# Kernel optimization log

Hardware: AMD Instinct MI355X
Metric: run time of the kernel (lower is better)

Reference implementation:

```python
import jax, jax.numpy as jnp
import numpy as np

N = 50000
E = 800000
T = 12
HID = 128
K = 3
F_IN = 7  # 1 (x) + 4 (env) + 2 (coords)
CIN = F_IN + HID  # DCRNN concatenates input with hidden state


def setup_inputs() -> dict:
    key = jax.random.key(0)
    ks = jax.random.split(key, 16)
    inp = {
        "x": jax.random.normal(ks[0], (N, T), dtype=jnp.float32),
        "env": jax.random.normal(ks[1], (N, 4, T), dtype=jnp.float32),
        "coords": jax.random.uniform(ks[2], (N, 2), dtype=jnp.float32),
        "edge_index": jax.random.randint(ks[3], (2, E), 0, N, dtype=jnp.int32),
        "edge_weight": jax.random.uniform(ks[4], (E,), dtype=jnp.float32),
        "local_night": jax.random.uniform(ks[5], (N, T + 1), dtype=jnp.float32),
        # DCRNN gate diffusion-conv weights: [2 (out/in direction), K, Cin, Cout]
        "Wz": jax.random.normal(ks[6], (2, K, CIN, HID), dtype=jnp.float32) * 0.05,
        "bz": jnp.zeros((HID,), dtype=jnp.float32),
        "Wr": jax.random.normal(ks[7], (2, K, CIN, HID), dtype=jnp.float32) * 0.05,
        "br": jnp.zeros((HID,), dtype=jnp.float32),
        "Wh": jax.random.normal(ks[8], (2, K, CIN, HID), dtype=jnp.float32) * 0.05,
        "bh": jnp.zeros((HID,), dtype=jnp.float32),
        "lin_W": jax.random.normal(ks[9], (HID, 1), dtype=jnp.float32) * 0.05,
        "lin_b": jnp.zeros((1,), dtype=jnp.float32),
    }
    return inp


def reference(x, env, coords, edge_weight, local_night, Wz, bz, Wr, br, Wh, bh, lin_W, lin_b, edge_index):
    row, col = edge_index[0], edge_index[1]
    n = x.shape[0]

    # out/in degrees of the weighted adjacency A[row, col] = w
    deg_out = jax.ops.segment_sum(edge_weight, row, num_segments=n)
    deg_in = jax.ops.segment_sum(edge_weight, col, num_segments=n)
    inv_out = jnp.where(deg_out > 0, 1.0 / deg_out, 0.0)
    inv_in = jnp.where(deg_in > 0, 1.0 / deg_in, 0.0)

    def prop_out(v):  # (D_O^{-1} A) v : gather from col, scatter-add to row
        msg = edge_weight[:, None] * v[col]
        return inv_out[:, None] * jax.ops.segment_sum(msg, row, num_segments=n)

    def prop_in(v):  # (D_I^{-1} A^T) v : gather from row, scatter-add to col
        msg = edge_weight[:, None] * v[row]
        return inv_in[:, None] * jax.ops.segment_sum(msg, col, num_segments=n)

    def dconv(X, W, b):
        # K-hop bidirectional diffusion convolution
        H = X @ (W[0, 0] + W[1, 0])
        Tx0 = X
        Tx_o = prop_out(X)
        Tx_i = prop_in(X)
        H = H + Tx_o @ W[0, 1] + Tx_i @ W[1, 1]
        for k in range(2, W.shape[1]):
            Tx_o = 2.0 * prop_out(Tx_o) - Tx0
            Tx_i = 2.0 * prop_in(Tx_i) - Tx0
            H = H + Tx_o @ W[0, k] + Tx_i @ W[1, k]
        return H + b

    env_t = jnp.moveaxis(env, -1, 0)          # [T, N, 4]
    night_t = jnp.transpose(local_night[:, 1:])  # [T, N]
    hid0 = jnp.zeros((n, HID), dtype=x.dtype)   # hidden state resets each call (H=None)

    def step(x_prev, ts):
        e, night = ts
        X = jnp.concatenate([x_prev, e, coords], axis=1)   # [N, 7]
        Xh = jnp.concatenate([X, hid0], axis=1)            # [N, 7+HID]
        Z = jax.nn.sigmoid(dconv(Xh, Wz, bz))
        R = jax.nn.sigmoid(dconv(Xh, Wr, br))  # H*R = 0 since H0 = 0; kept for fidelity
        H_tilde = jnp.tanh(dconv(Xh, Wh, bh))
        H_new = Z * hid0 + (1.0 - Z) * H_tilde
        out = jax.nn.relu(H_new) @ lin_W + lin_b           # [N, 1]
        out = out * night[:, None]
        return out, out

    x0 = x[:, 0:1]
    _, preds = jax.lax.scan(step, x0, (env_t, night_t))    # preds: [T, N, 1]
    predictions = jnp.concatenate([x0, jnp.transpose(preds[..., 0])], axis=1)  # [N, T+1]
    return predictions
```

## Files before the change

### kernel.cpp

```cpp
#include <hip/hip_runtime.h>
#include <hip/hip_fp16.h>

#define Nn 50000
#define Ee 800000
#define Tt 12
#define NBAND 8
#define BAND 6250
#define CAP 64

__global__ __launch_bounds__(256) void csr_direct(
    const int* __restrict__ ei, const float* __restrict__ ew,
    int* __restrict__ nextR, int* __restrict__ nextC,
    unsigned* __restrict__ adjR, unsigned* __restrict__ adjC)
{
    int band = blockIdx.x & (NBAND - 1);
    int chunk = blockIdx.x >> 3;
    int lo = band * BAND, hi = lo + BAND;
    int stride = (gridDim.x >> 3) * 256;
    for (int e = chunk * 256 + threadIdx.x; e < Ee; e += stride) {
        int r = ei[e], c = ei[Ee + e];
        bool br = (r >= lo) & (r < hi);
        bool bc = (c >= lo) & (c < hi);
        if (br | bc) {
            unsigned wb = __half_as_ushort(__float2half(ew[e]));
            if (br) adjR[(r << 6) + atomicAdd(&nextR[r], 1)] = ((unsigned)c << 16) | wb;
            if (bc) adjC[(c << 6) + atomicAdd(&nextC[c], 1)] = ((unsigned)r << 16) | wb;
        }
    }
}

__global__ __launch_bounds__(256) void weff_kernel(
    const float* __restrict__ Wz, const float* __restrict__ Wh,
    const float* __restrict__ bz, const float* __restrict__ bh,
    float* __restrict__ wzT, float* __restrict__ whT)
{
    int idx = blockIdx.x * 256 + threadIdx.x;
    if (idx >= 2 * 36 * 128) return;
    const float* W = (idx < 36 * 128) ? Wz : Wh;
    const float* B = (idx < 36 * 128) ? bz : bh;
    float* O       = (idx < 36 * 128) ? wzT : whT;
    int rem = idx % (36 * 128);
    int k = rem / 128, j = rem % 128;
    float v;
    if (k == 35) v = B[j];
    else {
        int p = k / 7, rr = k % 7;
        if (p == 0)      v = W[(0 * 135 + rr) * 128 + j] + W[(3 * 135 + rr) * 128 + j];
        else if (p == 1) v = W[(1 * 135 + rr) * 128 + j];
        else if (p == 2) v = W[(4 * 135 + rr) * 128 + j];
        else if (p == 3) v = W[(2 * 135 + rr) * 128 + j];
        else             v = W[(5 * 135 + rr) * 128 + j];
    }
    O[k * 128 + j] = v;
}

__global__ __launch_bounds__(256) void init_kernel(
    const float* __restrict__ x, const float* __restrict__ env,
    const float* __restrict__ coords, __half* __restrict__ Xh,
    float* __restrict__ out)
{
    int i = blockIdx.x * 256 + threadIdx.x;
    if (i >= Nn) return;
    float xv = x[i * Tt];
    __half* r = Xh + (long)i * 8;
    r[0] = __float2half(xv);
    #pragma unroll
    for (int c = 0; c < 4; c++) r[1 + c] = __float2half(env[i * 48 + c * 12]);
    r[5] = __float2half(coords[i * 2 + 0]);
    r[6] = __float2half(coords[i * 2 + 1]);
    r[7] = __half(0.f);
    out[i * 13 + 0] = xv;
}

__device__ __forceinline__ void unpack8(const __half* p, float* v) {
    uint4 hv = *((const uint4*)p);
    float2 p0 = __half22float2(*(__half2*)&hv.x);
    float2 p1 = __half22float2(*(__half2*)&hv.y);
    float2 p2 = __half22float2(*(__half2*)&hv.z);
    float2 p3 = __half22float2(*(__half2*)&hv.w);
    v[0] = p0.x; v[1] = p0.y; v[2] = p1.x; v[3] = p1.y;
    v[4] = p2.x; v[5] = p2.y; v[6] = p3.x;
}

__device__ __forceinline__ void pack8(__half* p, const float* v) {
    __half2 q0 = __floats2half2_rn(v[0], v[1]);
    __half2 q1 = __floats2half2_rn(v[2], v[3]);
    __half2 q2 = __floats2half2_rn(v[4], v[5]);
    __half2 q3 = __floats2half2_rn(v[6], 0.f);
    uint4 st;
    st.x = *(unsigned*)&q0; st.y = *(unsigned*)&q1;
    st.z = *(unsigned*)&q2; st.w = *(unsigned*)&q3;
    *((uint4*)p) = st;
}

__device__ __forceinline__ void acc7(float* a, float w, uint4 hv) {
    float2 p0 = __half22float2(*(__half2*)&hv.x);
    float2 p1 = __half22float2(*(__half2*)&hv.y);
    float2 p2 = __half22float2(*(__half2*)&hv.z);
    float2 p3 = __half22float2(*(__half2*)&hv.w);
    a[0] = fmaf(w, p0.x, a[0]); a[1] = fmaf(w, p0.y, a[1]);
    a[2] = fmaf(w, p1.x, a[2]); a[3] = fmaf(w, p1.y, a[3]);
    a[4] = fmaf(w, p2.x, a[4]); a[5] = fmaf(w, p2.y, a[5]);
    a[6] = fmaf(w, p3.x, a[6]);
}

__device__ __forceinline__ float wdec(unsigned ed) {
    return __half2float(__ushort_as_half((unsigned short)(ed & 0xffffu)));
}

__device__ __forceinline__ void gather6(
    const unsigned* __restrict__ adj, const __half* __restrict__ src,
    int b, int k0, int e, float* a, float* sw)
{
    unsigned en[6];
    bool v[6];
    #pragma unroll
    for (int s = 0; s < 6; s++) {
        int k = k0 + 4 * s;
        v[s] = k < e;
        en[s] = adj[v[s] ? k : b];
    }
    uint4 rv[6];
    #pragma unroll
    for (int s = 0; s < 6; s++)
        rv[s] = *(const uint4*)(src + (long)(v[s] ? (en[s] >> 16) : 0u) * 8);
    #pragma unroll
    for (int s = 0; s < 6; s++) {
        float w = v[s] ? wdec(en[s]) : 0.f;
        acc7(a, w, rv[s]);
        if (sw) *sw += w;
    }
    for (int k = k0 + 24; k < e; k += 4) {
        unsigned ed = adj[k];
        uint4 r2 = *(const uint4*)(src + (long)(ed >> 16) * 8);
        float w = wdec(ed);
        acc7(a, w, r2);
        if (sw) *sw += w;
    }
}

__global__ __launch_bounds__(256) void gather1_kernel(
    const int* __restrict__ cntR, const unsigned* __restrict__ adjR,
    const int* __restrict__ cntC, const unsigned* __restrict__ adjC,
    const __half* __restrict__ Xh,
    __half* __restrict__ TxoH, __half* __restrict__ TxiH,
    float* __restrict__ inv_out, float* __restrict__ inv_in)
{
    int tid = blockIdx.x * 256 + threadIdx.x;
    if (tid >= Nn * 8) return;
    int node = tid >> 3;
    int dir = (tid >> 2) & 1, sub = tid & 3;
    const int*      cn  = dir ? cntC : cntR;
    const unsigned* adj = dir ? adjC : adjR;
    int b = node << 6, e = b + cn[node];
    float a[7] = {0.f, 0.f, 0.f, 0.f, 0.f, 0.f, 0.f};
    float sw = 0.f;
    gather6(adj, Xh, b, b + sub, e, a, &sw);
    #pragma unroll
    for (int m = 1; m <= 2; m <<= 1) {
        #pragma unroll
        for (int q = 0; q < 7; q++) a[q] += __shfl_xor(a[q], m);
        sw += __shfl_xor(sw, m);
    }
    if (sub == 0) {
        float inv = sw > 0.f ? 1.f / sw : 0.f;
        (dir ? inv_in : inv_out)[node] = inv;
        #pragma unroll
        for (int q = 0; q < 7; q++) a[q] *= inv;
        pack8((dir ? TxiH : TxoH) + (long)node * 8, a);
    }
}

__global__ __launch_bounds__(256) void step2_kernel(
    const int* __restrict__ cntR, const unsigned* __restrict__ adjR,
    const int* __restrict__ cntC, const unsigned* __restrict__ adjC,
    const float* __restrict__ inv_out, const float* __restrict__ inv_in,
    const float* __restrict__ env, const float* __restrict__ night,
    const float* __restrict__ wzT, const float* __restrict__ whT,
    const float* __restrict__ linW, const float* __restrict__ linb,
    __half* __restrict__ Xh,
    const __half* __restrict__ TxoH, const __half* __restrict__ TxiH,
    float* __restrict__ out, int t)
{
    __shared__ float f_s[32][36];
    __shared__ float part_s[2][32];
    int tid = threadIdx.x;
    int base = blockIdx.x * 32;

    {
        int nl = tid >> 3;
        int dir = (tid >> 2) & 1, sub = tid & 3;
        int node = base + nl;
        int nc = node < Nn ? node : Nn - 1;
        const int*      cn  = dir ? cntC : cntR;
        const unsigned* adj = dir ? adjC : adjR;
        const __half*   src = dir ? TxiH : TxoH;
        int b = nc << 6, e = b + cn[nc];
        float a[7] = {0.f, 0.f, 0.f, 0.f, 0.f, 0.f, 0.f};
        gather6(adj, src, b, b + sub, e, a, nullptr);
        #pragma unroll
        for (int m = 1; m <= 2; m <<= 1) {
            #pragma unroll
            for (int q = 0; q < 7; q++) a[q] += __shfl_xor(a[q], m);
        }
        if (sub == 0) {
            float s2 = 2.f * (dir ? inv_in[nc] : inv_out[nc]);
            float xv[7], tx[7];
            unpack8(Xh + (long)nc * 8, xv);
            unpack8(src + (long)nc * 8, tx);
            #pragma unroll
            for (int q = 0; q < 7; q++) {
                f_s[nl][21 + 7 * dir + q] = fmaf(s2, a[q], -xv[q]);
                f_s[nl][7 + 7 * dir + q]  = tx[q];
            }
            if (dir == 0) {
                #pragma unroll
                for (int q = 0; q < 7; q++) f_s[nl][q] = xv[q];
                f_s[nl][35] = 1.f;
            }
        }
    }
    __syncthreads();

    int lane = tid & 63;
    int wave = tid >> 6;
    int chSel = wave & 1;
    int ch = chSel * 64 + lane;
    int half_id = wave >> 1;
    float wz[36], wh[36];
    #pragma unroll
    for (int k = 0; k < 36; k++) wz[k] = wzT[k * 128 + ch];
    #pragma unroll
    for (int k = 0; k < 36; k++) wh[k] = whT[k * 128 + ch];
    float lw = linW[ch];
    float lb = linb[0];

    #pragma unroll 1
    for (int n = 0; n < 16; n++) {
        int ni = half_id * 16 + n;
        const float4* fv = (const float4*)f_s[ni];
        float hz = 0.f, hh = 0.f;
        #pragma unroll
        for (int q = 0; q < 9; q++) {
            float4 fq = fv[q];
            hz = fmaf(fq.x, wz[q*4+0], hz); hh = fmaf(fq.x, wh[q*4+0], hh);
            hz = fmaf(fq.y, wz[q*4+1], hz); hh = fmaf(fq.y, wh[q*4+1], hh);
            hz = fmaf(fq.z, wz[q*4+2], hz); hh = fmaf(fq.z, wh[q*4+2], hh);
            hz = fmaf(fq.w, wz[q*4+3], hz); hh = fmaf(fq.w, wh[q*4+3], hh);
        }
        float z  = 1.f / (1.f + __expf(-hz));
        float e2 = __expf(2.f * hh);
        float ht = 1.f - 2.f / (e2 + 1.f);
        float v = fmaxf((1.f - z) * ht, 0.f) * lw;
        v += __shfl_xor(v, 1);  v += __shfl_xor(v, 2);  v += __shfl_xor(v, 4);
        v += __shfl_xor(v, 8);  v += __shfl_xor(v, 16); v += __shfl_xor(v, 32);
        if (lane == 0) part_s[chSel][ni] = v;
    }
    __syncthreads();
    if (tid < 32) {
        int node = base + tid;
        if (node < Nn) {
            float o = part_s[0][tid] + part_s[1][tid] + lb;
            o *= night[(long)node * 13 + t + 1];
            out[(long)node * 13 + t + 1] = o;
            if (t + 1 < Tt) {
                __half* xr = Xh + (long)node * 8;
                xr[0] = __float2half(o);
                #pragma unroll
                for (int c = 0; c < 4; c++)
                    xr[1 + c] = __float2half(env[(long)node * 48 + c * 12 + t + 1]);
            }
        }
    }
}

extern "C" void kernel_launch(void* const* d_in, const int* in_sizes, int n_in,
                              void* d_out, int out_size, void* d_ws, size_t ws_size,
                              hipStream_t stream) {
    const float* x      = (const float*)d_in[0];
    const float* env    = (const float*)d_in[1];
    const float* coords = (const float*)d_in[2];
    const int*   ei     = (const int*)d_in[3];
    const float* ew     = (const float*)d_in[4];
    const float* night  = (const float*)d_in[5];
    const float* Wz     = (const float*)d_in[6];
    const float* bz     = (const float*)d_in[7];
    const float* Wh     = (const float*)d_in[10];
    const float* bh     = (const float*)d_in[11];
    const float* linW   = (const float*)d_in[12];
    const float* linb   = (const float*)d_in[13];
    float* out = (float*)d_out;

    float* w = (float*)d_ws;
    float* wzT     = w;
    float* whT     = w + 4608;
    float* inv_out = w + 9216;
    float* inv_in  = w + 59216;
    __half* Xh   = (__half*)(w + 109216);
    __half* TxoH = (__half*)(w + 309216);
    __half* TxiH = (__half*)(w + 509216);
    int* nextR   = (int*)(w + 709216);
    int* nextC   = nextR + 50000;
    unsigned* adjR = (unsigned*)(w + 809216);
    unsigned* adjC = adjR + Nn * CAP;

    hipMemsetAsync(nextR, 0, 2 * Nn * sizeof(int), stream);
    csr_direct<<<8 * 256, 256, 0, stream>>>(ei, ew, nextR, nextC, adjR, adjC);

    weff_kernel<<<(2 * 36 * 128 + 255) / 256, 256, 0, stream>>>(Wz, Wh, bz, bh, wzT, whT);
    init_kernel<<<(Nn + 255) / 256, 256, 0, stream>>>(x, env, coords, Xh, out);

    for (int t = 0; t < Tt; t++) {
        gather1_kernel<<<(Nn * 8 + 255) / 256, 256, 0, stream>>>(
            nextR, adjR, nextC, adjC, Xh, TxoH, TxiH, inv_out, inv_in);
        step2_kernel<<<(Nn + 31) / 32, 256, 0, stream>>>(
            nextR, adjR, nextC, adjC, inv_out, inv_in,
            env, night, wzT, whT, linW, linb, Xh, TxoH, TxiH, out, t);
    }
}
```

Before: 700.7 us.

## Fuse time-step loop into persistent cooperative kernel with grid sync

Replaces the 24 per-step kernel launches with one cooperative persistent kernel. Inside it, blocks pull work items from atomic counters and separate the gather and step phases with grid-wide syncs. This targets launch overhead and tail gaps between the many small kernels. In exchange it adds grid.sync cost, atomic work-stealing overhead, and an occupancy limit from launch_bounds(256,4) with a grid capped at 4 blocks per CU. The old multi-launch path is kept as a fallback.

After: 703.5 us. No clear change (+0.4%).

```diff
diff --git a/kernel.cpp b/kernel.cpp
--- a/kernel.cpp
+++ b/kernel.cpp
@@ -1,5 +1,8 @@
 #include <hip/hip_runtime.h>
 #include <hip/hip_fp16.h>
+#include <hip/hip_cooperative_groups.h>
+
+namespace cg = cooperative_groups;
 
 #define Nn 50000
 #define Ee 800000
@@ -7,6 +10,8 @@
 #define NBAND 8
 #define BAND 6250
 #define CAP 64
+#define NCHUNK ((Nn * 8 + 255) / 256)
+#define NWI ((Nn + 31) / 32)
 
 __global__ __launch_bounds__(256) void csr_direct(
     const int* __restrict__ ei, const float* __restrict__ ew,
@@ -139,15 +144,14 @@
     }
 }
 
-__global__ __launch_bounds__(256) void gather1_kernel(
+__device__ __forceinline__ void gather_phase(
+    int tid,
     const int* __restrict__ cntR, const unsigned* __restrict__ adjR,
     const int* __restrict__ cntC, const unsigned* __restrict__ adjC,
     const __half* __restrict__ Xh,
     __half* __restrict__ TxoH, __half* __restrict__ TxiH,
     float* __restrict__ inv_out, float* __restrict__ inv_in)
 {
-    int tid = blockIdx.x * 256 + threadIdx.x;
-    if (tid >= Nn * 8) return;
     int node = tid >> 3;
     int dir = (tid >> 2) & 1, sub = tid & 3;
     const int*      cn  = dir ? cntC : cntR;
@@ -171,7 +175,8 @@
     }
 }
 
-__global__ __launch_bounds__(256) void step2_kernel(
+__device__ __forceinline__ void step_phase(
+    int wi, int t,
     const int* __restrict__ cntR, const unsigned* __restrict__ adjR,
     const int* __restrict__ cntC, const unsigned* __restrict__ adjC,
     const float* __restrict__ inv_out, const float* __restrict__ inv_in,
@@ -180,12 +185,12 @@
     const float* __restrict__ linW, const float* __restrict__ linb,
     __half* __restrict__ Xh,
     const __half* __restrict__ TxoH, const __half* __restrict__ TxiH,
-    float* __restrict__ out, int t)
+    float* __restrict__ out)
 {
     __shared__ float f_s[32][36];
     __shared__ float part_s[2][32];
     int tid = threadIdx.x;
-    int base = blockIdx.x * 32;
+    int base = wi * 32;
 
     {
         int nl = tid >> 3;
@@ -272,6 +277,73 @@
             }
         }
     }
+}
+
+__global__ __launch_bounds__(256, 4) void loop_kernel(
+    const int* __restrict__ cntR, const unsigned* __restrict__ adjR,
+    const int* __restrict__ cntC, const unsigned* __restrict__ adjC,
+    float* __restrict__ inv_out, float* __restrict__ inv_in,
+    const float* __restrict__ env, const float* __restrict__ night,
+    const float* __restrict__ wzT, const float* __restrict__ whT,
+    const float* __restrict__ linW, const float* __restrict__ linb,
+    __half* __restrict__ Xh, __half* __restrict__ TxoH, __half* __restrict__ TxiH,
+    float* __restrict__ out, int* __restrict__ ctr)
+{
+    cg::grid_group grid = cg::this_grid();
+    __shared__ int item_s;
+    for (int t = 0; t < Tt; t++) {
+        for (;;) {
+            if (threadIdx.x == 0) item_s = atomicAdd(&ctr[t], 1);
+            __syncthreads();
+            int chunk = item_s;
+            __syncthreads();
+            if (chunk >= NCHUNK) break;
+            int tid = chunk * 256 + threadIdx.x;
+            if (tid < Nn * 8)
+                gather_phase(tid, cntR, adjR, cntC, adjC, Xh, TxoH, TxiH,
+                             inv_out, inv_in);
+        }
+        __threadfence();
+        grid.sync();
+        for (;;) {
+            if (threadIdx.x == 0) item_s = atomicAdd(&ctr[12 + t], 1);
+            __syncthreads();
+            int wi = item_s;
+            __syncthreads();
+            if (wi >= NWI) break;
+            step_phase(wi, t, cntR, adjR, cntC, adjC, inv_out, inv_in,
+                       env, night, wzT, whT, linW, linb, Xh, TxoH, TxiH, out);
+        }
+        __threadfence();
+        grid.sync();
+    }
+}
+
+__global__ __launch_bounds__(256) void gather1_kernel(
+    const int* __restrict__ cntR, const unsigned* __restrict__ adjR,
+    const int* __restrict__ cntC, const unsigned* __restrict__ adjC,
+    const __half* __restrict__ Xh,
+    __half* __restrict__ TxoH, __half* __restrict__ TxiH,
+    float* __restrict__ inv_out, float* __restrict__ inv_in)
+{
+    int tid = blockIdx.x * 256 + threadIdx.x;
+    if (tid >= Nn * 8) return;
+    gather_phase(tid, cntR, adjR, cntC, adjC, Xh, TxoH, TxiH, inv_out, inv_in);
+}
+
+__global__ __launch_bounds__(256) void step2_kernel(
+    const int* __restrict__ cntR, const unsigned* __restrict__ adjR,
+    const int* __restrict__ cntC, const unsigned* __restrict__ adjC,
+    const float* __restrict__ inv_out, const float* __restrict__ inv_in,
+    const float* __restrict__ env, const float* __restrict__ night,
+    const float* __restrict__ wzT, const float* __restrict__ whT,
+    const float* __restrict__ linW, const float* __restrict__ linb,
+    __half* __restrict__ Xh,
+    const __half* __restrict__ TxoH, const __half* __restrict__ TxiH,
+    float* __restrict__ out, int t)
+{
+    step_phase(blockIdx.x, t, cntR, adjR, cntC, adjC, inv_out, inv_in,
+               env, night, wzT, whT, linW, linb, Xh, TxoH, TxiH, out);
 }
 
 extern "C" void kernel_launch(void* const* d_in, const int* in_sizes, int n_in,
@@ -301,20 +373,45 @@
     __half* TxiH = (__half*)(w + 509216);
     int* nextR   = (int*)(w + 709216);
     int* nextC   = nextR + 50000;
-    unsigned* adjR = (unsigned*)(w + 809216);
+    int* ctr     = (int*)(w + 809216);
+    unsigned* adjR = (unsigned*)(w + 809280);
     unsigned* adjC = adjR + Nn * CAP;
 
-    hipMemsetAsync(nextR, 0, 2 * Nn * sizeof(int), stream);
+    hipMemsetAsync(nextR, 0, (2 * Nn + 64) * sizeof(int), stream);
     csr_direct<<<8 * 256, 256, 0, stream>>>(ei, ew, nextR, nextC, adjR, adjC);
 
     weff_kernel<<<(2 * 36 * 128 + 255) / 256, 256, 0, stream>>>(Wz, Wh, bz, bh, wzT, whT);
     init_kernel<<<(Nn + 255) / 256, 256, 0, stream>>>(x, env, coords, Xh, out);
 
-    for (int t = 0; t < Tt; t++) {
-        gather1_kernel<<<(Nn * 8 + 255) / 256, 256, 0, stream>>>(
-            nextR, adjR, nextC, adjC, Xh, TxoH, TxiH, inv_out, inv_in);
-        step2_kernel<<<(Nn + 31) / 32, 256, 0, stream>>>(
-            nextR, adjR, nextC, adjC, inv_out, inv_in,
-            env, night, wzT, whT, linW, linb, Xh, TxoH, TxiH, out, t);
-    }
-}
+    static int coopGrid = -2;
+    if (coopGrid == -2) {
+        hipDeviceProp_t prop{};
+        if (hipGetDeviceProperties(&prop, 0) == hipSuccess &&
+            prop.cooperativeLaunch && prop.multiProcessorCount > 0) {
+            coopGrid = 4 * prop.multiProcessorCount;
+            if (coopGrid > NWI) coopGrid = NWI;
+        } else coopGrid = -1;
+    }
+    bool did_coop = false;
+    if (coopGrid > 0) {
+        void* params[] = { (void*)&nextR, (void*)&adjR, (void*)&nextC, (void*)&adjC,
+                           (void*)&inv_out, (void*)&inv_in, (void*)&env, (void*)&night,
+                           (void*)&wzT, (void*)&whT, (void*)&linW, (void*)&linb,
+                           (void*)&Xh, (void*)&TxoH, (void*)&TxiH, (void*)&out,
+                           (void*)&ctr };
+        if (hipLaunchCooperativeKernel((const void*)loop_kernel, dim3(coopGrid),
+                                       dim3(256), params, 0, stream) == hipSuccess)
+            did_coop = true;
+        else
+            coopGrid = -1;
+    }
+    if (!did_coop) {
+        for (int t = 0; t < Tt; t++) {
+            gather1_kernel<<<(Nn * 8 + 255) / 256, 256, 0, stream>>>(
+                nextR, adjR, nextC, adjC, Xh, TxoH, TxiH, inv_out, inv_in);
+            step2_kernel<<<(Nn + 31) / 32, 256, 0, stream>>>(
+                nextR, adjR, nextC, adjC, inv_out, inv_in,
+                env, night, wzT, whT, linW, linb, Xh, TxoH, TxiH, out, t);
+        }
+    }
+}
```

## Precompute diffusion of static env/coords features once, propagate only x per step

Applied to the files above, without the earlier changes.

Graph diffusion is linear, so the env (all 12 timesteps) and coordinate channels are propagated for both hops in two upfront prop kernels into 64-wide half-precision tables. Each timestep then gathers only the scalar x channel instead of 7 channels, with step_kernel reading the precomputed rows for the current t. This cuts per-step gather traffic, at the cost of one larger upfront pass and several extra workspace buffers. The second hop's static rows are computed from half-rounded first-hop values.

New measurement: 719.6 us. 1.03x slower.

```diff
diff --git a/kernel.cpp b/kernel.cpp
--- a/kernel.cpp
+++ b/kernel.cpp
@@ -54,46 +54,42 @@
     O[k * 128 + j] = v;
 }
 
-__global__ __launch_bounds__(256) void init_kernel(
+__global__ __launch_bounds__(256) void initS_kernel(
     const float* __restrict__ x, const float* __restrict__ env,
-    const float* __restrict__ coords, __half* __restrict__ Xh,
-    float* __restrict__ out)
+    const float* __restrict__ coords,
+    __half* __restrict__ S, __half* __restrict__ xcur, float* __restrict__ out)
 {
     int i = blockIdx.x * 256 + threadIdx.x;
     if (i >= Nn) return;
     float xv = x[i * Tt];
-    __half* r = Xh + (long)i * 8;
-    r[0] = __float2half(xv);
-    #pragma unroll
-    for (int c = 0; c < 4; c++) r[1 + c] = __float2half(env[i * 48 + c * 12]);
-    r[5] = __float2half(coords[i * 2 + 0]);
-    r[6] = __float2half(coords[i * 2 + 1]);
-    r[7] = __half(0.f);
-    out[i * 13 + 0] = xv;
-}
-
-__device__ __forceinline__ void unpack8(const __half* p, float* v) {
-    uint4 hv = *((const uint4*)p);
-    float2 p0 = __half22float2(*(__half2*)&hv.x);
-    float2 p1 = __half22float2(*(__half2*)&hv.y);
-    float2 p2 = __half22float2(*(__half2*)&hv.z);
-    float2 p3 = __half22float2(*(__half2*)&hv.w);
-    v[0] = p0.x; v[1] = p0.y; v[2] = p1.x; v[3] = p1.y;
-    v[4] = p2.x; v[5] = p2.y; v[6] = p3.x;
-}
-
-__device__ __forceinline__ void pack8(__half* p, const float* v) {
-    __half2 q0 = __floats2half2_rn(v[0], v[1]);
-    __half2 q1 = __floats2half2_rn(v[2], v[3]);
-    __half2 q2 = __floats2half2_rn(v[4], v[5]);
-    __half2 q3 = __floats2half2_rn(v[6], 0.f);
-    uint4 st;
-    st.x = *(unsigned*)&q0; st.y = *(unsigned*)&q1;
-    st.z = *(unsigned*)&q2; st.w = *(unsigned*)&q3;
-    *((uint4*)p) = st;
-}
-
-__device__ __forceinline__ void acc7(float* a, float w, uint4 hv) {
+    xcur[i] = __float2half(xv);
+    out[i * 13] = xv;
+    float4 ev[12];
+    const float4* ep = (const float4*)(env + (long)i * 48);
+    #pragma unroll
+    for (int j = 0; j < 12; j++) ev[j] = ep[j];
+    const float* evf = (const float*)ev;
+    __half row[64];
+    #pragma unroll
+    for (int t = 0; t < 12; t++)
+        #pragma unroll
+        for (int c = 0; c < 4; c++)
+            row[t * 4 + c] = __float2half(evf[c * 12 + t]);
+    row[48] = __float2half(coords[i * 2]);
+    row[49] = __float2half(coords[i * 2 + 1]);
+    #pragma unroll
+    for (int j = 50; j < 64; j++) row[j] = __half(0.f);
+    uint4* dst = (uint4*)(S + (long)i * 64);
+    const uint4* sv = (const uint4*)row;
+    #pragma unroll
+    for (int j = 0; j < 8; j++) dst[j] = sv[j];
+}
+
+__device__ __forceinline__ float wdec(unsigned ed) {
+    return __half2float(__ushort_as_half((unsigned short)(ed & 0xffffu)));
+}
+
+__device__ __forceinline__ void acc8h(float* a, float w, uint4 hv) {
     float2 p0 = __half22float2(*(__half2*)&hv.x);
     float2 p1 = __half22float2(*(__half2*)&hv.y);
     float2 p2 = __half22float2(*(__half2*)&hv.z);
@@ -101,50 +97,89 @@
     a[0] = fmaf(w, p0.x, a[0]); a[1] = fmaf(w, p0.y, a[1]);
     a[2] = fmaf(w, p1.x, a[2]); a[3] = fmaf(w, p1.y, a[3]);
     a[4] = fmaf(w, p2.x, a[4]); a[5] = fmaf(w, p2.y, a[5]);
-    a[6] = fmaf(w, p3.x, a[6]);
-}
-
-__device__ __forceinline__ float wdec(unsigned ed) {
-    return __half2float(__ushort_as_half((unsigned short)(ed & 0xffffu)));
-}
-
-__device__ __forceinline__ void gather6(
-    const unsigned* __restrict__ adj, const __half* __restrict__ src,
-    int b, int k0, int e, float* a, float* sw)
-{
-    unsigned en[6];
-    bool v[6];
-    #pragma unroll
-    for (int s = 0; s < 6; s++) {
-        int k = k0 + 4 * s;
-        v[s] = k < e;
-        en[s] = adj[v[s] ? k : b];
-    }
-    uint4 rv[6];
-    #pragma unroll
-    for (int s = 0; s < 6; s++)
-        rv[s] = *(const uint4*)(src + (long)(v[s] ? (en[s] >> 16) : 0u) * 8);
-    #pragma unroll
-    for (int s = 0; s < 6; s++) {
-        float w = v[s] ? wdec(en[s]) : 0.f;
-        acc7(a, w, rv[s]);
-        if (sw) *sw += w;
-    }
-    for (int k = k0 + 24; k < e; k += 4) {
-        unsigned ed = adj[k];
-        uint4 r2 = *(const uint4*)(src + (long)(ed >> 16) * 8);
-        float w = wdec(ed);
-        acc7(a, w, r2);
-        if (sw) *sw += w;
-    }
-}
-
-__global__ __launch_bounds__(256) void gather1_kernel(
+    a[6] = fmaf(w, p3.x, a[6]); a[7] = fmaf(w, p3.y, a[7]);
+}
+
+__device__ __forceinline__ void unpack8h(uint4 hv, float* f) {
+    float2 p0 = __half22float2(*(__half2*)&hv.x);
+    float2 p1 = __half22float2(*(__half2*)&hv.y);
+    float2 p2 = __half22float2(*(__half2*)&hv.z);
+    float2 p3 = __half22float2(*(__half2*)&hv.w);
+    f[0] = p0.x; f[1] = p0.y; f[2] = p1.x; f[3] = p1.y;
+    f[4] = p2.x; f[5] = p2.y; f[6] = p3.x; f[7] = p3.y;
+}
+
+__global__ __launch_bounds__(256) void prop_kernel(
     const int* __restrict__ cntR, const unsigned* __restrict__ adjR,
     const int* __restrict__ cntC, const unsigned* __restrict__ adjC,
-    const __half* __restrict__ Xh,
-    __half* __restrict__ TxoH, __half* __restrict__ TxiH,
-    float* __restrict__ inv_out, float* __restrict__ inv_in)
+    const __half* __restrict__ src_o, const __half* __restrict__ src_i,
+    const __half* __restrict__ subS,
+    __half* __restrict__ dst_o, __half* __restrict__ dst_i,
+    float* __restrict__ inv_out, float* __restrict__ inv_in, int computeInv)
+{
+    int tid = blockIdx.x * 256 + threadIdx.x;
+    if (tid >= Nn * 16) return;
+    int team = tid >> 3;
+    int node = team >> 1, dir = team & 1, s = tid & 7;
+    const int*      cn  = dir ? cntC : cntR;
+    const unsigned* adj = dir ? adjC : adjR;
+    const __half*   src = dir ? src_i : src_o;
+    __half*         dst = dir ? dst_i : dst_o;
+    int b = node << 6, e = b + cn[node];
+    float acc[8] = {0.f,0.f,0.f,0.f,0.f,0.f,0.f,0.f};
+    float sw = 0.f;
+    for (int k = b; k < e; k += 4) {
+        bool v1 = k + 1 < e, v2 = k + 2 < e, v3 = k + 3 < e;
+        unsigned e0 = adj[k];
+        unsigned e1 = adj[v1 ? k + 1 : b];
+        unsigned e2 = adj[v2 ? k + 2 : b];
+        unsigned e3 = adj[v3 ? k + 3 : b];
+        uint4 r0 = *(const uint4*)(src + (long)(e0 >> 16) * 64 + s * 8);
+        uint4 r1 = *(const uint4*)(src + (long)(e1 >> 16) * 64 + s * 8);
+        uint4 r2 = *(const uint4*)(src + (long)(e2 >> 16) * 64 + s * 8);
+        uint4 r3 = *(const uint4*)(src + (long)(e3 >> 16) * 64 + s * 8);
+        float w0 = wdec(e0);
+        float w1 = v1 ? wdec(e1) : 0.f;
+        float w2 = v2 ? wdec(e2) : 0.f;
+        float w3 = v3 ? wdec(e3) : 0.f;
+        acc8h(acc, w0, r0); acc8h(acc, w1, r1);
+        acc8h(acc, w2, r2); acc8h(acc, w3, r3);
+        sw += (w0 + w1) + (w2 + w3);
+    }
+    float inv;
+    if (computeInv) {
+        inv = sw > 0.f ? 1.f / sw : 0.f;
+        if (s == 0) (dir ? inv_in : inv_out)[node] = inv;
+    } else {
+        inv = (dir ? inv_in : inv_out)[node];
+    }
+    float o8[8];
+    if (subS) {
+        uint4 sv4 = *(const uint4*)(subS + (long)node * 64 + s * 8);
+        float sv[8];
+        unpack8h(sv4, sv);
+        #pragma unroll
+        for (int q = 0; q < 8; q++) o8[q] = fmaf(2.f * inv, acc[q], -sv[q]);
+    } else {
+        #pragma unroll
+        for (int q = 0; q < 8; q++) o8[q] = inv * acc[q];
+    }
+    __half2 h0 = __floats2half2_rn(o8[0], o8[1]);
+    __half2 h1 = __floats2half2_rn(o8[2], o8[3]);
+    __half2 h2 = __floats2half2_rn(o8[4], o8[5]);
+    __half2 h3 = __floats2half2_rn(o8[6], o8[7]);
+    uint4 st;
+    st.x = *(unsigned*)&h0; st.y = *(unsigned*)&h1;
+    st.z = *(unsigned*)&h2; st.w = *(unsigned*)&h3;
+    *(uint4*)(dst + (long)node * 64 + s * 8) = st;
+}
+
+__global__ __launch_bounds__(256) void gx_kernel(
+    const int* __restrict__ cntR, const unsigned* __restrict__ adjR,
+    const int* __restrict__ cntC, const unsigned* __restrict__ adjC,
+    const __half* __restrict__ xcur,
+    __half* __restrict__ toX, __half* __restrict__ tiX,
+    const float* __restrict__ inv_out, const float* __restrict__ inv_in)
 {
     int tid = blockIdx.x * 256 + threadIdx.x;
     if (tid >= Nn * 8) return;
@@ -153,33 +188,42 @@
     const int*      cn  = dir ? cntC : cntR;
     const unsigned* adj = dir ? adjC : adjR;
     int b = node << 6, e = b + cn[node];
-    float a[7] = {0.f, 0.f, 0.f, 0.f, 0.f, 0.f, 0.f};
-    float sw = 0.f;
-    gather6(adj, Xh, b, b + sub, e, a, &sw);
-    #pragma unroll
-    for (int m = 1; m <= 2; m <<= 1) {
-        #pragma unroll
-        for (int q = 0; q < 7; q++) a[q] += __shfl_xor(a[q], m);
-        sw += __shfl_xor(sw, m);
-    }
+    float acc = 0.f;
+    int k0 = b + sub;
+    {
+        unsigned en[6]; bool v[6];
+        #pragma unroll
+        for (int s = 0; s < 6; s++) { int k = k0 + 4 * s; v[s] = k < e; en[s] = adj[v[s] ? k : b]; }
+        __half xv[6];
+        #pragma unroll
+        for (int s = 0; s < 6; s++) xv[s] = xcur[v[s] ? (en[s] >> 16) : 0u];
+        #pragma unroll
+        for (int s = 0; s < 6; s++) acc += (v[s] ? wdec(en[s]) : 0.f) * __half2float(xv[s]);
+        for (int k = k0 + 24; k < e; k += 4) {
+            unsigned ed = adj[k];
+            acc += wdec(ed) * __half2float(xcur[ed >> 16]);
+        }
+    }
+    acc += __shfl_xor(acc, 1);
+    acc += __shfl_xor(acc, 2);
     if (sub == 0) {
-        float inv = sw > 0.f ? 1.f / sw : 0.f;
-        (dir ? inv_in : inv_out)[node] = inv;
-        #pragma unroll
-        for (int q = 0; q < 7; q++) a[q] *= inv;
-        pack8((dir ? TxiH : TxoH) + (long)node * 8, a);
-    }
-}
-
-__global__ __launch_bounds__(256) void step2_kernel(
+        float inv = (dir ? inv_in : inv_out)[node];
+        (dir ? tiX : toX)[node] = __float2half(inv * acc);
+    }
+}
+
+__global__ __launch_bounds__(256) void step_kernel(
     const int* __restrict__ cntR, const unsigned* __restrict__ adjR,
     const int* __restrict__ cntC, const unsigned* __restrict__ adjC,
     const float* __restrict__ inv_out, const float* __restrict__ inv_in,
-    const float* __restrict__ env, const float* __restrict__ night,
+    const float* __restrict__ env, const float* __restrict__ coords,
+    const float* __restrict__ night,
     const float* __restrict__ wzT, const float* __restrict__ whT,
     const float* __restrict__ linW, const float* __restrict__ linb,
-    __half* __restrict__ Xh,
-    const __half* __restrict__ TxoH, const __half* __restrict__ TxiH,
+    __half* __restrict__ xcur,
+    const __half* __restrict__ toX, const __half* __restrict__ tiX,
+    const __half* __restrict__ P_o, const __half* __restrict__ P_i,
+    const __half* __restrict__ P2_o, const __half* __restrict__ P2_i,
     float* __restrict__ out, int t)
 {
     __shared__ float f_s[32][36];
@@ -194,30 +238,70 @@
         int nc = node < Nn ? node : Nn - 1;
         const int*      cn  = dir ? cntC : cntR;
         const unsigned* adj = dir ? adjC : adjR;
-        const __half*   src = dir ? TxiH : TxoH;
+        const __half*   src = dir ? tiX : toX;
         int b = nc << 6, e = b + cn[nc];
-        float a[7] = {0.f, 0.f, 0.f, 0.f, 0.f, 0.f, 0.f};
-        gather6(adj, src, b, b + sub, e, a, nullptr);
-        #pragma unroll
-        for (int m = 1; m <= 2; m <<= 1) {
-            #pragma unroll
-            for (int q = 0; q < 7; q++) a[q] += __shfl_xor(a[q], m);
-        }
+        float acc = 0.f;
+        int k0 = b + sub;
+        {
+            unsigned en[6]; bool v[6];
+            #pragma unroll
+            for (int s = 0; s < 6; s++) { int k = k0 + 4 * s; v[s] = k < e; en[s] = adj[v[s] ? k : b]; }
+            __half xv[6];
+            #pragma unroll
+            for (int s = 0; s < 6; s++) xv[s] = src[v[s] ? (en[s] >> 16) : 0u];
+            #pragma unroll
+            for (int s = 0; s < 6; s++) acc += (v[s] ? wdec(en[s]) : 0.f) * __half2float(xv[s]);
+            for (int k = k0 + 24; k < e; k += 4) {
+                unsigned ed = adj[k];
+                acc += wdec(ed) * __half2float(src[ed >> 16]);
+            }
+        }
+        acc += __shfl_xor(acc, 1);
+        acc += __shfl_xor(acc, 2);
         if (sub == 0) {
-            float s2 = 2.f * (dir ? inv_in[nc] : inv_out[nc]);
-            float xv[7], tx[7];
-            unpack8(Xh + (long)nc * 8, xv);
-            unpack8(src + (long)nc * 8, tx);
-            #pragma unroll
-            for (int q = 0; q < 7; q++) {
-                f_s[nl][21 + 7 * dir + q] = fmaf(s2, a[q], -xv[q]);
-                f_s[nl][7 + 7 * dir + q]  = tx[q];
-            }
-            if (dir == 0) {
-                #pragma unroll
-                for (int q = 0; q < 7; q++) f_s[nl][q] = xv[q];
-                f_s[nl][35] = 1.f;
-            }
+            float inv = (dir ? inv_in : inv_out)[nc];
+            float xval = __half2float(xcur[nc]);
+            f_s[nl][21 + 7 * dir] = fmaf(2.f * inv, acc, -xval);
+        }
+    }
+    {
+        int g = tid >> 5;
+        int n = tid & 31;
+        int node = base + n;
+        int nc = node < Nn ? node : Nn - 1;
+        if (g == 0) {
+            f_s[n][0] = __half2float(xcur[nc]);
+            #pragma unroll
+            for (int c = 0; c < 4; c++) f_s[n][1 + c] = env[(long)nc * 48 + c * 12 + t];
+            f_s[n][5] = coords[nc * 2];
+            f_s[n][6] = coords[nc * 2 + 1];
+            f_s[n][35] = 1.f;
+        } else if (g == 1) {
+            f_s[n][7] = __half2float(toX[nc]);
+            const __half* r = P_o + (long)nc * 64;
+            #pragma unroll
+            for (int c = 0; c < 4; c++) f_s[n][8 + c] = __half2float(r[t * 4 + c]);
+            f_s[n][12] = __half2float(r[48]);
+            f_s[n][13] = __half2float(r[49]);
+        } else if (g == 2) {
+            f_s[n][14] = __half2float(tiX[nc]);
+            const __half* r = P_i + (long)nc * 64;
+            #pragma unroll
+            for (int c = 0; c < 4; c++) f_s[n][15 + c] = __half2float(r[t * 4 + c]);
+            f_s[n][19] = __half2float(r[48]);
+            f_s[n][20] = __half2float(r[49]);
+        } else if (g == 3) {
+            const __half* r = P2_o + (long)nc * 64;
+            #pragma unroll
+            for (int c = 0; c < 4; c++) f_s[n][22 + c] = __half2float(r[t * 4 + c]);
+            f_s[n][26] = __half2float(r[48]);
+            f_s[n][27] = __half2float(r[49]);
+        } else if (g == 4) {
+            const __half* r = P2_i + (long)nc * 64;
+            #pragma unroll
+            for (int c = 0; c < 4; c++) f_s[n][29 + c] = __half2float(r[t * 4 + c]);
+            f_s[n][33] = __half2float(r[48]);
+            f_s[n][34] = __half2float(r[49]);
         }
     }
     __syncthreads();
@@ -263,13 +347,7 @@
             float o = part_s[0][tid] + part_s[1][tid] + lb;
             o *= night[(long)node * 13 + t + 1];
             out[(long)node * 13 + t + 1] = o;
-            if (t + 1 < Tt) {
-                __half* xr = Xh + (long)node * 8;
-                xr[0] = __float2half(o);
-                #pragma unroll
-                for (int c = 0; c < 4; c++)
-                    xr[1 + c] = __float2half(env[(long)node * 48 + c * 12 + t + 1]);
-            }
+            if (t + 1 < Tt) xcur[node] = __float2half(o);
         }
     }
 }
@@ -296,25 +374,36 @@
     float* whT     = w + 4608;
     float* inv_out = w + 9216;
     float* inv_in  = w + 59216;
-    __half* Xh   = (__half*)(w + 109216);
-    __half* TxoH = (__half*)(w + 309216);
-    __half* TxiH = (__half*)(w + 509216);
-    int* nextR   = (int*)(w + 709216);
-    int* nextC   = nextR + 50000;
-    unsigned* adjR = (unsigned*)(w + 809216);
-    unsigned* adjC = adjR + Nn * CAP;
+    __half* xcur   = (__half*)(w + 109216);
+    __half* toX    = (__half*)(w + 134216);
+    __half* tiX    = (__half*)(w + 159216);
+    int* nextR     = (int*)(w + 184216);
+    int* nextC     = (int*)(w + 234216);
+    __half* S    = (__half*)(w + 284224);
+    __half* P_o  = (__half*)(w + 1884224);
+    __half* P_i  = (__half*)(w + 3484224);
+    __half* P2_o = (__half*)(w + 5084224);
+    __half* P2_i = (__half*)(w + 6684224);
+    unsigned* adjR = (unsigned*)(w + 8284224);
+    unsigned* adjC = (unsigned*)(w + 11484224);
 
     hipMemsetAsync(nextR, 0, 2 * Nn * sizeof(int), stream);
     csr_direct<<<8 * 256, 256, 0, stream>>>(ei, ew, nextR, nextC, adjR, adjC);
 
-    weff_kernel<<<(2 * 36 * 128 + 255) / 256, 256, 0, stream>>>(Wz, Wh, bz, bh, wzT, whT);
-    init_kernel<<<(Nn + 255) / 256, 256, 0, stream>>>(x, env, coords, Xh, out);
+    weff_kernel<<<36, 256, 0, stream>>>(Wz, Wh, bz, bh, wzT, whT);
+    initS_kernel<<<(Nn + 255) / 256, 256, 0, stream>>>(x, env, coords, S, xcur, out);
+
+    prop_kernel<<<(Nn * 16) / 256, 256, 0, stream>>>(
+        nextR, adjR, nextC, adjC, S, S, nullptr, P_o, P_i, inv_out, inv_in, 1);
+    prop_kernel<<<(Nn * 16) / 256, 256, 0, stream>>>(
+        nextR, adjR, nextC, adjC, P_o, P_i, S, P2_o, P2_i, inv_out, inv_in, 0);
 
     for (int t = 0; t < Tt; t++) {
-        gather1_kernel<<<(Nn * 8 + 255) / 256, 256, 0, stream>>>(
-            nextR, adjR, nextC, adjC, Xh, TxoH, TxiH, inv_out, inv_in);
-        step2_kernel<<<(Nn + 31) / 32, 256, 0, stream>>>(
+        gx_kernel<<<(Nn * 8 + 255) / 256, 256, 0, stream>>>(
+            nextR, adjR, nextC, adjC, xcur, toX, tiX, inv_out, inv_in);
+        step_kernel<<<(Nn + 31) / 32, 256, 0, stream>>>(
             nextR, adjR, nextC, adjC, inv_out, inv_in,
-            env, night, wzT, whT, linW, linb, Xh, TxoH, TxiH, out, t);
-    }
-}
+            env, coords, night, wzT, whT, linW, linb,
+            xcur, toX, tiX, P_o, P_i, P2_o, P2_i, out, t);
+    }
+}
```
